# Kernel optimization log

Hardware: AMD Instinct MI355X
Metric: run time of the kernel (lower is better)

## Reference

```python
import jax, jax.numpy as jnp
import numpy as np

WIDTH = [512, 512, 512, 512]
GRID_SIZE = 5
K = 3  # spline order
GRID_RANGE = (-1.0, 1.0)
BATCH = 1024


def extend_grid(grid, k):
    # grid: (I, G+1) -> (I, G+2k+1), extend k knots on each side with uniform step h
    h = (grid[:, -1:] - grid[:, :1]) / (grid.shape[1] - 1)
    for _ in range(k):
        grid = jnp.concatenate([grid[:, :1] - h, grid, grid[:, -1:] + h], axis=1)
    return grid


def b_spline_basis(x, grid, k):
    # Cox-de Boor recursion. x: (B, I), grid: (I, G+2k+1) -> (B, I, G+k)
    xe = x[:, :, None]
    g = grid[None, :, :]
    B = ((xe >= g[:, :, :-1]) & (xe < g[:, :, 1:])).astype(x.dtype)
    for p in range(1, k + 1):
        B = ((xe - g[:, :, :-(p + 1)]) / (g[:, :, p:-1] - g[:, :, :-(p + 1)]) * B[:, :, :-1]
             + (g[:, :, p + 1:] - xe) / (g[:, :, p + 1:] - g[:, :, 1:-p]) * B[:, :, 1:])
    return B


def kan_layer(x, grid, coef, sb, sp):
    # x: (B, I); coef: (I, O, G+k); sb, sp: (I, O)
    base = jax.nn.silu(x)                              # residual b(x), (B, I)
    Bmat = b_spline_basis(x, grid, K)                  # (B, I, G+k)
    y = jnp.einsum('bik,iok->bio', Bmat, coef)         # spline curves, (B, I, O)
    post = sb[None] * base[:, :, None] + sp[None] * y  # postacts (B, I, O)
    return post.sum(axis=1)                            # (B, O)


def setup_inputs() -> dict:
    key = jax.random.key(0)
    ks = jax.random.split(key, 1 + 2 * (len(WIDTH) - 1))
    inp = {"x": jax.random.normal(ks[0], (BATCH, WIDTH[0]), dtype=jnp.float32)}
    for l, (i, o) in enumerate(zip(WIDTH[:-1], WIDTH[1:])):
        base = jnp.linspace(GRID_RANGE[0], GRID_RANGE[1], GRID_SIZE + 1, dtype=jnp.float32)
        grid = extend_grid(jnp.broadcast_to(base[None], (i, GRID_SIZE + 1)), K)
        kc, kb = ks[1 + 2 * l], ks[2 + 2 * l]
        inp[f"grid{l}"] = grid
        inp[f"coef{l}"] = jax.random.normal(kc, (i, o, GRID_SIZE + K), dtype=jnp.float32) * (0.1 / GRID_SIZE)
        inp[f"sb{l}"] = (jax.random.uniform(kb, (i, o), dtype=jnp.float32) * 2.0 - 1.0) / np.sqrt(i).astype(np.float32)
        inp[f"sp{l}"] = jnp.ones((i, o), dtype=jnp.float32) / np.sqrt(i).astype(np.float32)
    return inp


def reference(x, grid0, coef0, sb0, sp0, grid1, coef1, sb1, sp1, grid2, coef2, sb2, sp2):
    x = kan_layer(x, grid0, coef0, sb0, sp0)
    x = kan_layer(x, grid1, coef1, sb1, sp1)
    x = kan_layer(x, grid2, coef2, sb2, sp2)
    return x
```

## Files before the change

kernel.cpp:

```cpp
#include <hip/hip_runtime.h>
#include <hip/hip_bf16.h>

#define I_DIM  512
#define O_DIM  512
#define NBATCH 1024
#define NSPL   8
#define KPI    12
#define KDIM   (I_DIM * KPI)
#define NGRID  12

#define SPLITK 4
#define KSEG   (KDIM / SPLITK)
#define BK     64
#define BM     64
#define BN     64

typedef __attribute__((ext_vector_type(8))) short bf16x8;
typedef __attribute__((ext_vector_type(4))) float f32x4;

__device__ __forceinline__ void gload_lds16(const __hip_bfloat16* g, __hip_bfloat16* l) {
    __builtin_amdgcn_global_load_lds(
        (const __attribute__((address_space(1))) void*)g,
        (__attribute__((address_space(3))) void*)l, 16, 0, 0);
}

__device__ __forceinline__ void features_core(float xv, const float* __restrict__ grid,
                                              int i, __hip_bfloat16* __restrict__ dst) {
    float g[NGRID];
#pragma unroll
    for (int j = 0; j < NGRID; ++j) g[j] = grid[i * NGRID + j];

    float B[NGRID - 1];
#pragma unroll
    for (int j = 0; j < NGRID - 1; ++j)
        B[j] = (xv >= g[j] && xv < g[j + 1]) ? 1.0f : 0.0f;
#pragma unroll
    for (int p = 1; p <= 3; ++p) {
#pragma unroll
        for (int j = 0; j < NGRID - 1 - p; ++j) {
            B[j] = (xv - g[j]) / (g[j + p] - g[j]) * B[j]
                 + (g[j + p + 1] - xv) / (g[j + p + 1] - g[j + 1]) * B[j + 1];
        }
    }
    float s = xv / (1.0f + __expf(-xv));
    __hip_bfloat16 shi = __float2bfloat16(s);
    __hip_bfloat16 slo = __float2bfloat16(s - __bfloat162float(shi));

    __align__(16) __hip_bfloat16 row[KPI];
#pragma unroll
    for (int k = 0; k < NSPL; ++k) row[k] = __float2bfloat16(B[k]);
    row[8]  = shi;
    row[9]  = shi;
    row[10] = slo;
    row[11] = __float2bfloat16(0.0f);

    uint2* d = (uint2*)dst;
    const uint2* srow = (const uint2*)row;
    d[0] = srow[0]; d[1] = srow[1]; d[2] = srow[2];
}

__device__ __forceinline__ void wt_row_core(const float* __restrict__ coef,
                                            const float* __restrict__ sb,
                                            const float* __restrict__ sp,
                                            int i, int o,
                                            __hip_bfloat16* __restrict__ W) {
    float sbv = sb[i * O_DIM + o];
    float spv = sp[i * O_DIM + o];
    const float* cf = coef + (size_t)(i * O_DIM + o) * NSPL;
    __align__(16) __hip_bfloat16 row[KPI];
#pragma unroll
    for (int k = 0; k < NSPL; ++k) row[k] = __float2bfloat16(spv * cf[k]);
    __hip_bfloat16 whi = __float2bfloat16(sbv);
    __hip_bfloat16 wlo = __float2bfloat16(sbv - __bfloat162float(whi));
    row[8]  = whi;
    row[9]  = wlo;
    row[10] = whi;
    row[11] = __float2bfloat16(0.0f);
    uint2* dst = (uint2*)(W + (size_t)o * KDIM + i * KPI);
    const uint2* src = (const uint2*)row;
    dst[0] = src[0]; dst[1] = src[1]; dst[2] = src[2];
}

#define WT_BLOCKS   3072
#define FEAT_BLOCKS 2048
__global__ __launch_bounds__(256)
void prep_kernel(const float* __restrict__ x0, const float* __restrict__ gr0,
                 const float* __restrict__ c0, const float* __restrict__ sb0, const float* __restrict__ sp0,
                 const float* __restrict__ c1, const float* __restrict__ sb1, const float* __restrict__ sp1,
                 const float* __restrict__ c2, const float* __restrict__ sb2, const float* __restrict__ sp2,
                 __hip_bfloat16* __restrict__ Wt,
                 __hip_bfloat16* __restrict__ F) {
    int b = blockIdx.x;
    int t = threadIdx.x;
    if (b < WT_BLOCKS) {
        int l   = b >> 10;
        int rem = b & 1023;
        int i0  = (rem & 7) * 64;
        int o0  = (rem >> 3) * 4;
        const float* coef = l == 0 ? c0  : (l == 1 ? c1  : c2);
        const float* sb   = l == 0 ? sb0 : (l == 1 ? sb1 : sb2);
        const float* sp   = l == 0 ? sp0 : (l == 1 ? sp1 : sp2);
        wt_row_core(coef, sb, sp, i0 + (t >> 2), o0 + (t & 3),
                    Wt + (size_t)l * O_DIM * KDIM);
    } else {
        int e = (b - WT_BLOCKS) * 256 + t;
        features_core(x0[e], gr0, e & (I_DIM - 1), F + (size_t)e * KPI);
    }
}

__global__ __launch_bounds__(256)
void build_features_sum(const float* __restrict__ P,
                        const float* __restrict__ grid,
                        __hip_bfloat16* __restrict__ F) {
    int tid = blockIdx.x * blockDim.x + threadIdx.x;
    float xv = 0.f;
#pragma unroll
    for (int s = 0; s < SPLITK; ++s) xv += P[(size_t)s * NBATCH * I_DIM + tid];
    features_core(xv, grid, tid & (I_DIM - 1), F + (size_t)tid * KPI);
}

__global__ __launch_bounds__(256)
void reduce_out(const float* __restrict__ P, float* __restrict__ out) {
    int tid = blockIdx.x * blockDim.x + threadIdx.x;
    float v = 0.f;
#pragma unroll
    for (int s = 0; s < SPLITK; ++s) v += P[(size_t)s * NBATCH * O_DIM + tid];
    out[tid] = v;
}

__global__ __launch_bounds__(256)
void gemm_kernel(const __hip_bfloat16* __restrict__ A,
                 const __hip_bfloat16* __restrict__ Wt,
                 float* __restrict__ P) {
    __shared__ __hip_bfloat16 lA[BM * BK];
    __shared__ __hip_bfloat16 lB[BN * BK];

    int bm = blockIdx.x;
    int bn = blockIdx.y;
    int ks = blockIdx.z;
    int tid = threadIdx.x;
    int lane = tid & 63;
    int wave = tid >> 6;
    int wr = (wave & 1) * 32;
    int wc = (wave >> 1) * 32;
    int q  = lane >> 4;
    int ln = lane & 15;

    f32x4 acc[2][2];
#pragma unroll
    for (int a = 0; a < 2; ++a)
#pragma unroll
        for (int b = 0; b < 2; ++b) acc[a][b] = (f32x4){0.f, 0.f, 0.f, 0.f};

    const __hip_bfloat16* Abase = A  + (size_t)(bm * BM) * KDIM + ks * KSEG;
    const __hip_bfloat16* Bbase = Wt + (size_t)(bn * BN) * KDIM + ks * KSEG;

    for (int kt = 0; kt < KSEG; kt += BK) {
        __syncthreads();
#pragma unroll
        for (int c = 0; c < 2; ++c) {
            int cc = wave * 128 + c * 64 + lane;
            int r = cc >> 3, j = (cc & 7) ^ (r & 7);
            gload_lds16(Abase + (size_t)r * KDIM + kt + j * 8,
                        lA + (size_t)(wave * 128 + c * 64) * 8);
        }
#pragma unroll
        for (int c = 0; c < 2; ++c) {
            int cc = wave * 128 + c * 64 + lane;
            int r = cc >> 3, j = (cc & 7) ^ (r & 7);
            gload_lds16(Bbase + (size_t)r * KDIM + kt + j * 8,
                        lB + (size_t)(wave * 128 + c * 64) * 8);
        }
        __syncthreads();

#pragma unroll
        for (int kh = 0; kh < 2; ++kh) {
            bf16x8 af[2], bfr[2];
#pragma unroll
            for (int rt = 0; rt < 2; ++rt) {
                int row = wr + rt * 16 + ln;
                af[rt] = *(const bf16x8*)(lA + row * BK + (((kh * 4 + q) ^ (row & 7)) * 8));
            }
#pragma unroll
            for (int ct = 0; ct < 2; ++ct) {
                int row = wc + ct * 16 + ln;
                bfr[ct] = *(const bf16x8*)(lB + row * BK + (((kh * 4 + q) ^ (row & 7)) * 8));
            }
#pragma unroll
            for (int rt = 0; rt < 2; ++rt)
#pragma unroll
                for (int ct = 0; ct < 2; ++ct)
                    acc[rt][ct] = __builtin_amdgcn_mfma_f32_16x16x32_bf16(
                        af[rt], bfr[ct], acc[rt][ct], 0, 0, 0);
        }
    }

    float* Pp = P + (size_t)ks * NBATCH * O_DIM;
    int orow = bm * BM + wr;
    int ocol = bn * BN + wc + ln;
#pragma unroll
    for (int rt = 0; rt < 2; ++rt)
#pragma unroll
        for (int ct = 0; ct < 2; ++ct)
#pragma unroll
            for (int r = 0; r < 4; ++r)
                Pp[(size_t)(orow + rt * 16 + q * 4 + r) * O_DIM + ocol + ct * 16]
                    = acc[rt][ct][r];
}

extern "C" void kernel_launch(void* const* d_in, const int* in_sizes, int n_in,
                              void* d_out, int out_size, void* d_ws, size_t ws_size,
                              hipStream_t stream) {
    const float* x0  = (const float*)d_in[0];
    const float* gr0 = (const float*)d_in[1];
    const float* c0  = (const float*)d_in[2];
    const float* sb0 = (const float*)d_in[3];
    const float* sp0 = (const float*)d_in[4];
    const float* gr1 = (const float*)d_in[5];
    const float* c1  = (const float*)d_in[6];
    const float* sb1 = (const float*)d_in[7];
    const float* sp1 = (const float*)d_in[8];
    const float* gr2 = (const float*)d_in[9];
    const float* c2  = (const float*)d_in[10];
    const float* sb2 = (const float*)d_in[11];
    const float* sp2 = (const float*)d_in[12];

    char* ws = (char*)d_ws;
    const size_t wt_bytes = (size_t)O_DIM * KDIM * sizeof(__hip_bfloat16);
    const size_t f_bytes  = (size_t)NBATCH * KDIM * sizeof(__hip_bfloat16);
    __hip_bfloat16* Wt = (__hip_bfloat16*)ws;
    __hip_bfloat16* F  = (__hip_bfloat16*)(ws + 3 * wt_bytes);
    float* P = (float*)(ws + 3 * wt_bytes + f_bytes);
    float* out = (float*)d_out;

    prep_kernel<<<WT_BLOCKS + FEAT_BLOCKS, 256, 0, stream>>>(
        x0, gr0, c0, sb0, sp0, c1, sb1, sp1, c2, sb2, sp2, Wt, F);

    gemm_kernel<<<dim3(NBATCH / BM, O_DIM / BN, SPLITK), 256, 0, stream>>>(F, Wt, P);

    build_features_sum<<<(NBATCH * I_DIM) / 256, 256, 0, stream>>>(P, gr1, F);
    gemm_kernel<<<dim3(NBATCH / BM, O_DIM / BN, SPLITK), 256, 0, stream>>>(
        F, Wt + (size_t)O_DIM * KDIM, P);

    build_features_sum<<<(NBATCH * I_DIM) / 256, 256, 0, stream>>>(P, gr2, F);
    gemm_kernel<<<dim3(NBATCH / BM, O_DIM / BN, SPLITK), 256, 0, stream>>>(
        F, Wt + (size_t)2 * O_DIM * KDIM, P);

    reduce_out<<<(NBATCH * O_DIM) / 256, 256, 0, stream>>>(P, out);
}
```

Measured before the change: 199.9 us.

## Double-buffer LDS tiles in split-K GEMM to overlap loads with MFMA

Splits the LDS A/B tiles into two buffers and prefetches the next K tile with global_load_lds while MFMAs run on the current one. This cuts one barrier per tile and hides part of the global-memory latency. It doubles LDS use per block, which may lower occupancy. Correctness depends on the async LDS loads being complete at the barrier; NT is 24, so the even-count loop is exact.

```diff
diff --git a/kernel.cpp b/kernel.cpp
--- a/kernel.cpp
+++ b/kernel.cpp
@@ -14,6 +14,7 @@
 #define BK     64
 #define BM     64
 #define BN     64
+#define NT     (KSEG / BK)
 
 typedef __attribute__((ext_vector_type(8))) short bf16x8;
 typedef __attribute__((ext_vector_type(4))) float f32x4;
@@ -132,8 +133,8 @@
 void gemm_kernel(const __hip_bfloat16* __restrict__ A,
                  const __hip_bfloat16* __restrict__ Wt,
                  float* __restrict__ P) {
-    __shared__ __hip_bfloat16 lA[BM * BK];
-    __shared__ __hip_bfloat16 lB[BN * BK];
+    __shared__ __hip_bfloat16 lA[2][BM * BK];
+    __shared__ __hip_bfloat16 lB[2][BN * BK];
 
     int bm = blockIdx.x;
     int bn = blockIdx.y;
@@ -155,45 +156,62 @@
     const __hip_bfloat16* Abase = A  + (size_t)(bm * BM) * KDIM + ks * KSEG;
     const __hip_bfloat16* Bbase = Wt + (size_t)(bn * BN) * KDIM + ks * KSEG;
 
-    for (int kt = 0; kt < KSEG; kt += BK) {
+    int cc0 = wave * 128 + lane;
+    int cc1 = cc0 + 64;
+    int r0 = cc0 >> 3, j0 = (cc0 & 7) ^ (r0 & 7);
+    int r1 = cc1 >> 3, j1 = (cc1 & 7) ^ (r1 & 7);
+    size_t offA0 = (size_t)r0 * KDIM + j0 * 8;
+    size_t offA1 = (size_t)r1 * KDIM + j1 * 8;
+    int ldst0 = (wave * 128) * 8;
+    int ldst1 = (wave * 128 + 64) * 8;
+
+#define STAGE(buf, kt)                                                        \
+    do {                                                                      \
+        gload_lds16(Abase + offA0 + (kt), &lA[buf][ldst0]);                   \
+        gload_lds16(Abase + offA1 + (kt), &lA[buf][ldst1]);                   \
+        gload_lds16(Bbase + offA0 + (kt), &lB[buf][ldst0]);                   \
+        gload_lds16(Bbase + offA1 + (kt), &lB[buf][ldst1]);                   \
+    } while (0)
+
+#define COMPUTE(buf)                                                          \
+    do {                                                                      \
+        _Pragma("unroll")                                                     \
+        for (int kh = 0; kh < 2; ++kh) {                                      \
+            bf16x8 af[2], bfr[2];                                             \
+            _Pragma("unroll")                                                 \
+            for (int rt = 0; rt < 2; ++rt) {                                  \
+                int row = wr + rt * 16 + ln;                                  \
+                af[rt] = *(const bf16x8*)(&lA[buf][0] + row * BK +            \
+                                          (((kh * 4 + q) ^ (row & 7)) * 8));  \
+            }                                                                 \
+            _Pragma("unroll")                                                 \
+            for (int ct = 0; ct < 2; ++ct) {                                  \
+                int row = wc + ct * 16 + ln;                                  \
+                bfr[ct] = *(const bf16x8*)(&lB[buf][0] + row * BK +           \
+                                           (((kh * 4 + q) ^ (row & 7)) * 8)); \
+            }                                                                 \
+            _Pragma("unroll")                                                 \
+            for (int rt = 0; rt < 2; ++rt)                                    \
+                _Pragma("unroll")                                             \
+                for (int ct = 0; ct < 2; ++ct)                                \
+                    acc[rt][ct] = __builtin_amdgcn_mfma_f32_16x16x32_bf16(    \
+                        af[rt], bfr[ct], acc[rt][ct], 0, 0, 0);               \
+        }                                                                     \
+    } while (0)
+
+    STAGE(0, 0);
+    __syncthreads();
+
+    for (int t = 0; t < NT; t += 2) {
+        STAGE(1, (t + 1) * BK);
+        COMPUTE(0);
         __syncthreads();
-#pragma unroll
-        for (int c = 0; c < 2; ++c) {
-            int cc = wave * 128 + c * 64 + lane;
-            int r = cc >> 3, j = (cc & 7) ^ (r & 7);
-            gload_lds16(Abase + (size_t)r * KDIM + kt + j * 8,
-                        lA + (size_t)(wave * 128 + c * 64) * 8);
-        }
-#pragma unroll
-        for (int c = 0; c < 2; ++c) {
-            int cc = wave * 128 + c * 64 + lane;
-            int r = cc >> 3, j = (cc & 7) ^ (r & 7);
-            gload_lds16(Bbase + (size_t)r * KDIM + kt + j * 8,
-                        lB + (size_t)(wave * 128 + c * 64) * 8);
-        }
+        if (t + 2 < NT) STAGE(0, (t + 2) * BK);
+        COMPUTE(1);
         __syncthreads();
-
-#pragma unroll
-        for (int kh = 0; kh < 2; ++kh) {
-            bf16x8 af[2], bfr[2];
-#pragma unroll
-            for (int rt = 0; rt < 2; ++rt) {
-                int row = wr + rt * 16 + ln;
-                af[rt] = *(const bf16x8*)(lA + row * BK + (((kh * 4 + q) ^ (row & 7)) * 8));
-            }
-#pragma unroll
-            for (int ct = 0; ct < 2; ++ct) {
-                int row = wc + ct * 16 + ln;
-                bfr[ct] = *(const bf16x8*)(lB + row * BK + (((kh * 4 + q) ^ (row & 7)) * 8));
-            }
-#pragma unroll
-            for (int rt = 0; rt < 2; ++rt)
-#pragma unroll
-                for (int ct = 0; ct < 2; ++ct)
-                    acc[rt][ct] = __builtin_amdgcn_mfma_f32_16x16x32_bf16(
-                        af[rt], bfr[ct], acc[rt][ct], 0, 0, 0);
-        }
     }
+#undef STAGE
+#undef COMPUTE
 
     float* Pp = P + (size_t)ks * NBATCH * O_DIM;
     int orow = bm * BM + wr;
```

Result: slower. 213.1 us (+6.6%).

## Fuse split-K reduction and next-layer feature build into GEMM epilogue

Applied to the files above, without the earlier changes.

Each GEMM tile now increments a per-tile atomic counter after writing its split-K partial, and the last-arriving block sums the partials and directly builds the next layer's bf16 spline features (or writes the final output). This removes the separate build_features_sum and reduce_out kernels and their launches. It also uses three separate feature buffers so a layer's GEMM never overwrites the input it is still reading. The cost is extra workspace, threadfence/atomic synchronisation, and a serialized epilogue done only by the winning block.

```diff
diff --git a/kernel.cpp b/kernel.cpp
--- a/kernel.cpp
+++ b/kernel.cpp
@@ -83,15 +83,19 @@
 
 #define WT_BLOCKS   3072
 #define FEAT_BLOCKS 2048
+#define NCTR        (3 * 128)
 __global__ __launch_bounds__(256)
 void prep_kernel(const float* __restrict__ x0, const float* __restrict__ gr0,
                  const float* __restrict__ c0, const float* __restrict__ sb0, const float* __restrict__ sp0,
                  const float* __restrict__ c1, const float* __restrict__ sb1, const float* __restrict__ sp1,
                  const float* __restrict__ c2, const float* __restrict__ sb2, const float* __restrict__ sp2,
                  __hip_bfloat16* __restrict__ Wt,
-                 __hip_bfloat16* __restrict__ F) {
+                 __hip_bfloat16* __restrict__ F0,
+                 int* __restrict__ ctr) {
     int b = blockIdx.x;
     int t = threadIdx.x;
+    int z = b * 256 + t;
+    if (z < NCTR) ctr[z] = 0;
     if (b < WT_BLOCKS) {
         int l   = b >> 10;
         int rem = b & 1023;
@@ -104,36 +108,22 @@
                     Wt + (size_t)l * O_DIM * KDIM);
     } else {
         int e = (b - WT_BLOCKS) * 256 + t;
-        features_core(x0[e], gr0, e & (I_DIM - 1), F + (size_t)e * KPI);
+        features_core(x0[e], gr0, e & (I_DIM - 1), F0 + (size_t)e * KPI);
     }
 }
 
 __global__ __launch_bounds__(256)
-void build_features_sum(const float* __restrict__ P,
-                        const float* __restrict__ grid,
-                        __hip_bfloat16* __restrict__ F) {
-    int tid = blockIdx.x * blockDim.x + threadIdx.x;
-    float xv = 0.f;
-#pragma unroll
-    for (int s = 0; s < SPLITK; ++s) xv += P[(size_t)s * NBATCH * I_DIM + tid];
-    features_core(xv, grid, tid & (I_DIM - 1), F + (size_t)tid * KPI);
-}
-
-__global__ __launch_bounds__(256)
-void reduce_out(const float* __restrict__ P, float* __restrict__ out) {
-    int tid = blockIdx.x * blockDim.x + threadIdx.x;
-    float v = 0.f;
-#pragma unroll
-    for (int s = 0; s < SPLITK; ++s) v += P[(size_t)s * NBATCH * O_DIM + tid];
-    out[tid] = v;
-}
-
-__global__ __launch_bounds__(256)
-void gemm_kernel(const __hip_bfloat16* __restrict__ A,
-                 const __hip_bfloat16* __restrict__ Wt,
-                 float* __restrict__ P) {
+void gemm_fused(const __hip_bfloat16* __restrict__ A,
+                const __hip_bfloat16* __restrict__ Wt,
+                float* __restrict__ P,
+                const float* __restrict__ grid_next,
+                __hip_bfloat16* __restrict__ Fn,
+                float* __restrict__ out,
+                int last,
+                int* __restrict__ ctr) {
     __shared__ __hip_bfloat16 lA[BM * BK];
     __shared__ __hip_bfloat16 lB[BN * BK];
+    __shared__ int win;
 
     int bm = blockIdx.x;
     int bn = blockIdx.y;
@@ -206,6 +196,31 @@
             for (int r = 0; r < 4; ++r)
                 Pp[(size_t)(orow + rt * 16 + q * 4 + r) * O_DIM + ocol + ct * 16]
                     = acc[rt][ct][r];
+
+    __syncthreads();
+    if (tid == 0) {
+        __threadfence();
+        int old = atomicAdd(&ctr[bm * 8 + bn], 1);
+        win = (old == SPLITK - 1);
+    }
+    __syncthreads();
+    if (win) {
+        __threadfence();
+#pragma unroll
+        for (int it = 0; it < 16; ++it) {
+            int p = it * 256 + tid;
+            int b = bm * BM + (p >> 6);
+            int o = bn * BN + (p & 63);
+            float xv = 0.f;
+#pragma unroll
+            for (int s = 0; s < SPLITK; ++s)
+                xv += P[(size_t)s * NBATCH * O_DIM + (size_t)b * O_DIM + o];
+            if (!last)
+                features_core(xv, grid_next, o, Fn + (size_t)b * KDIM + o * KPI);
+            else
+                out[(size_t)b * O_DIM + o] = xv;
+        }
+    }
 }
 
 extern "C" void kernel_launch(void* const* d_in, const int* in_sizes, int n_in,
@@ -229,22 +244,20 @@
     const size_t wt_bytes = (size_t)O_DIM * KDIM * sizeof(__hip_bfloat16);
     const size_t f_bytes  = (size_t)NBATCH * KDIM * sizeof(__hip_bfloat16);
     __hip_bfloat16* Wt = (__hip_bfloat16*)ws;
-    __hip_bfloat16* F  = (__hip_bfloat16*)(ws + 3 * wt_bytes);
-    float* P = (float*)(ws + 3 * wt_bytes + f_bytes);
+    __hip_bfloat16* F0 = (__hip_bfloat16*)(ws + 3 * wt_bytes);
+    __hip_bfloat16* F1 = F0 + (size_t)NBATCH * KDIM;
+    __hip_bfloat16* F2 = F1 + (size_t)NBATCH * KDIM;
+    float* P  = (float*)(ws + 3 * wt_bytes + 3 * f_bytes);
+    int* ctr  = (int*)(P + (size_t)SPLITK * NBATCH * O_DIM);
     float* out = (float*)d_out;
 
     prep_kernel<<<WT_BLOCKS + FEAT_BLOCKS, 256, 0, stream>>>(
-        x0, gr0, c0, sb0, sp0, c1, sb1, sp1, c2, sb2, sp2, Wt, F);
-
-    gemm_kernel<<<dim3(NBATCH / BM, O_DIM / BN, SPLITK), 256, 0, stream>>>(F, Wt, P);
-
-    build_features_sum<<<(NBATCH * I_DIM) / 256, 256, 0, stream>>>(P, gr1, F);
-    gemm_kernel<<<dim3(NBATCH / BM, O_DIM / BN, SPLITK), 256, 0, stream>>>(
-        F, Wt + (size_t)O_DIM * KDIM, P);
-
-    build_features_sum<<<(NBATCH * I_DIM) / 256, 256, 0, stream>>>(P, gr2, F);
-    gemm_kernel<<<dim3(NBATCH / BM, O_DIM / BN, SPLITK), 256, 0, stream>>>(
-        F, Wt + (size_t)2 * O_DIM * KDIM, P);
-
-    reduce_out<<<(NBATCH * O_DIM) / 256, 256, 0, stream>>>(P, out);
-}
+        x0, gr0, c0, sb0, sp0, c1, sb1, sp1, c2, sb2, sp2, Wt, F0, ctr);
+
+    dim3 gg(NBATCH / BM, O_DIM / BN, SPLITK);
+    gemm_fused<<<gg, 256, 0, stream>>>(F0, Wt, P, gr1, F1, out, 0, ctr);
+    gemm_fused<<<gg, 256, 0, stream>>>(F1, Wt + (size_t)O_DIM * KDIM, P,
+                                       gr2, F2, out, 0, ctr + 128);
+    gemm_fused<<<gg, 256, 0, stream>>>(F2, Wt + (size_t)2 * O_DIM * KDIM, P,
+                                       nullptr, nullptr, out, 1, ctr + 256);
+}
```

After: 321.3 us. 60.7% more time.
